# Performance work log

Hardware: AMD Instinct MI355X
Metric: run time of the kernel (lower is better)

## Reference

```python
import jax, jax.numpy as jnp
import numpy as np

L, E, S, V, B, T = 6, 768, 1024, 32000, 2, 1024
FF = 4 * E
EPS = 1e-5

def _layernorm(v, w, b):
    m = jnp.mean(v, axis=-1, keepdims=True)
    var = jnp.mean((v - m) ** 2, axis=-1, keepdims=True)
    return (v - m) * jax.lax.rsqrt(var + EPS) * w + b

def setup_inputs() -> dict:
    key = jax.random.key(0)
    ks = jax.random.split(key, 12)
    s = 0.02
    n = lambda k, shp: (jax.random.normal(k, shp, jnp.float32) * s)
    return {
        "x": jax.random.randint(ks[0], (B, T), 0, V),
        "tok_emb": n(ks[1], (V, E)),
        "pos_emb": jax.random.normal(ks[2], (S, E), jnp.float32),  # nn.Parameter(randn)
        "Wq": n(ks[3], (L, E, E)), "bq": jnp.zeros((L, E), jnp.float32),
        "Wk": n(ks[4], (L, E, E)), "bk": jnp.zeros((L, E), jnp.float32),
        "Wv": n(ks[5], (L, E, E)), "bv": jnp.zeros((L, E), jnp.float32),
        "ln1w": jnp.ones((L, E), jnp.float32), "ln1b": jnp.zeros((L, E), jnp.float32),
        "W1": n(ks[6], (L, E, FF)), "b1": jnp.zeros((L, FF), jnp.float32),
        "W2": n(ks[7], (L, FF, E)), "b2": jnp.zeros((L, E), jnp.float32),
        "ln2w": jnp.ones((L, E), jnp.float32), "ln2b": jnp.zeros((L, E), jnp.float32),
        "Wo": n(ks[8], (E, V)), "bo": jnp.zeros((V,), jnp.float32),
    }

def reference(x, tok_emb, pos_emb, Wq, bq, Wk, bk, Wv, bv, ln1w, ln1b,
              W1, b1, W2, b2, ln2w, ln2b, Wo, bo):
    t = x.shape[1]
    h = tok_emb[x] + pos_emb[:t]  # [B,T,E]
    scale = jnp.sqrt(jnp.float32(E))
    tril = jnp.tril(jnp.ones((t, t), bool))

    def layer(h, p):
        wq, bq_, wk, bk_, wv, bv_, l1w, l1b, w1, b1_, w2, b2_, l2w, l2b = p
        Q = h @ wq + bq_
        K = h @ wk + bk_
        Vv = h @ wv + bv_
        scores = jnp.einsum('btd,bsd->bts', Q, K) / scale
        # original adds a mask of 1.0 on allowed positions, -inf elsewhere
        masked = jnp.where(tril, scores + 1.0, -jnp.inf)
        A = jax.nn.softmax(masked, axis=-1)
        att = jnp.einsum('bts,bsd->btd', A, Vv)
        h1 = _layernorm(h + att, l1w, l1b)
        ffn = jax.nn.relu(h1 @ w1 + b1_) @ w2 + b2_
        h2 = _layernorm(ffn + h1, l2w, l2b)
        return h2, None

    params = (Wq, bq, Wk, bk, Wv, bv, ln1w, ln1b, W1, b1, W2, b2, ln2w, ln2b)
    h, _ = jax.lax.scan(layer, h, params)
    return h @ Wo + bo  # [B,T,V]
```

## Files before the change

kernel.cpp:

```cpp
#include <hip/hip_runtime.h>
#include <stdint.h>

typedef __bf16 v8bf __attribute__((ext_vector_type(8)));
typedef float  v4f  __attribute__((ext_vector_type(4)));

__device__ __forceinline__ float bf2f(uint16_t h) {
    union { uint32_t u; float f; } x; x.u = ((uint32_t)h) << 16; return x.f;
}
__device__ __forceinline__ uint16_t f2bf(float f) {
    union { float f; uint32_t u; } x; x.f = f;
    uint32_t r = x.u + 0x7fffu + ((x.u >> 16) & 1u);
    return (uint16_t)(r >> 16);
}

__device__ __forceinline__ void gload16(const uint16_t* g, uint16_t* l) {
    __builtin_amdgcn_global_load_lds((const __attribute__((address_space(1))) void*)g,
                                     (__attribute__((address_space(3))) void*)l, 16, 0, 0);
}

__global__ void k_embed(const int* __restrict__ x, const float* __restrict__ tok,
                        const float* __restrict__ pos, float* __restrict__ hf,
                        uint16_t* __restrict__ hb)
{
    int i = blockIdx.x;
    int t = i & 1023;
    int tk = x[i];
    const float* te = tok + (long)tk * 768;
    const float* pe = pos + (long)t * 768;
    for (int j = threadIdx.x; j < 768; j += 256) {
        float v = te[j] + pe[j];
        hf[(long)i * 768 + j] = v;
        hb[(long)i * 768 + j] = f2bf(v);
    }
}

template<typename SrcT>
__global__ void k_transpose(const SrcT* __restrict__ src, uint16_t* __restrict__ dst,
                            int ldS, int ldD, long sBatch, long dBatch)
{
    __shared__ float tile[32][33];
    src += (long)blockIdx.z * sBatch;
    dst += (long)blockIdx.z * dBatch;
    int c0 = blockIdx.x * 32, r0 = blockIdx.y * 32;
    int tx = threadIdx.x, ty = threadIdx.y;
    #pragma unroll
    for (int i = 0; i < 4; ++i) {
        int r = r0 + ty + i * 8;
        SrcT s = src[(long)r * ldS + c0 + tx];
        float v;
        if constexpr (sizeof(SrcT) == 4) v = (float)s; else v = bf2f((uint16_t)s);
        tile[ty + i * 8][tx] = v;
    }
    __syncthreads();
    #pragma unroll
    for (int i = 0; i < 4; ++i) {
        int c = c0 + ty + i * 8;
        dst[(long)c * ldD + r0 + tx] = f2bf(tile[tx][ty + i * 8]);
    }
}

__global__ void k_concat3(const float* __restrict__ a, const float* __restrict__ b,
                          const float* __restrict__ c, float* __restrict__ out)
{
    int l = blockIdx.y;
    const float* s = (blockIdx.x == 0) ? a : ((blockIdx.x == 1) ? b : c);
    s += (long)l * 768;
    for (int j = threadIdx.x; j < 768; j += 256)
        out[(long)l * 2304 + blockIdx.x * 768 + j] = s[j];
}

template<typename OutT, int BN, bool BIAS, bool RELU, bool RES>
__global__ void k_gemm(const uint16_t* __restrict__ A, const uint16_t* __restrict__ BT,
                       OutT* __restrict__ C, const float* __restrict__ bias,
                       const float* __restrict__ res,
                       int K, int lda, int ldb, int ldc,
                       long bsA, long bsB, long bsC, float scale, int causal)
{
    constexpr int NT = BN / 32;
    const int nwg = gridDim.x * gridDim.y;
    int lin = blockIdx.y * gridDim.x + blockIdx.x;
    {
        int q = nwg >> 3, r = nwg & 7, x = lin & 7, i = lin >> 3;
        lin = (x < r ? x * (q + 1) : r * (q + 1) + (x - r) * q) + i;
    }
    const int mt = lin % gridDim.y;
    const int nt = lin / gridDim.y;

    if (causal == 1 && nt * BN >= (mt + 1) * 128) return;
    const int Keff = (causal == 2) ? ((mt + 1) * 128 < K ? (mt + 1) * 128 : K) : K;

    __shared__ uint16_t As[128 * 32];
    __shared__ uint16_t Bs[BN * 32];
    const int tid  = threadIdx.x;
    const int lane = tid & 63;
    const int bz   = blockIdx.z;
    const uint16_t* Ab = A + (long)bz * bsA + (long)mt * 128 * lda;
    const uint16_t* Bb = BT + (long)bz * bsB + (long)nt * BN * ldb;

    const int wm = (tid >> 6) >> 1, wn = (tid >> 6) & 1;
    const int fr = lane & 15, fq = lane >> 4;

    const int r0 = tid >> 2;
    const int s0 = (tid & 3) * 8;

    v4f acc[4][NT];
    #pragma unroll
    for (int m = 0; m < 4; ++m)
        #pragma unroll
        for (int n = 0; n < NT; ++n) acc[m][n] = (v4f){0.f, 0.f, 0.f, 0.f};

    for (int kt = 0; kt < Keff; kt += 32) {
        gload16(Ab + (long)r0 * lda + kt + s0,        &As[tid * 8]);
        gload16(Ab + (long)(r0 + 64) * lda + kt + s0, &As[2048 + tid * 8]);
        gload16(Bb + (long)r0 * ldb + kt + s0,        &Bs[tid * 8]);
        if constexpr (BN == 128)
            gload16(Bb + (long)(r0 + 64) * ldb + kt + s0, &Bs[2048 + tid * 8]);
        __syncthreads();
        v8bf ag[4], bg[NT];
        #pragma unroll
        for (int m = 0; m < 4; ++m)
            ag[m] = *(const v8bf*)&As[(wm * 64 + m * 16 + fr) * 32 + fq * 8];
        #pragma unroll
        for (int n = 0; n < NT; ++n)
            bg[n] = *(const v8bf*)&Bs[(wn * (BN / 2) + n * 16 + fr) * 32 + fq * 8];
        #pragma unroll
        for (int m = 0; m < 4; ++m)
            #pragma unroll
            for (int n = 0; n < NT; ++n)
                acc[m][n] = __builtin_amdgcn_mfma_f32_16x16x32_bf16(ag[m], bg[n], acc[m][n], 0, 0, 0);
        __syncthreads();
    }

    OutT* Cb = C + (long)bz * bsC + (long)mt * 128 * ldc + nt * BN;
    const float* Rb = RES ? (res + (long)bz * bsC + (long)mt * 128 * ldc + nt * BN) : nullptr;
    #pragma unroll
    for (int n = 0; n < NT; ++n) {
        int col = wn * (BN / 2) + n * 16 + fr;
        float bv = BIAS ? bias[nt * BN + col] : 0.f;
        #pragma unroll
        for (int m = 0; m < 4; ++m) {
            #pragma unroll
            for (int r = 0; r < 4; ++r) {
                int row = wm * 64 + m * 16 + fq * 4 + r;
                float v = acc[m][n][r] * scale + bv;
                if (RES) v += Rb[(long)row * ldc + col];
                if (RELU) v = fmaxf(v, 0.f);
                if constexpr (sizeof(OutT) == 4) Cb[(long)row * ldc + col] = v;
                else                             Cb[(long)row * ldc + col] = f2bf(v);
            }
        }
    }
}

__global__ void k_softmax(const float* __restrict__ S, uint16_t* __restrict__ P)
{
    int t = blockIdx.x, b = blockIdx.y;
    const float* row = S + ((long)b * 1024 + t) * 1024;
    uint16_t* pr = P + ((long)b * 1024 + t) * 1024;
    int limit = (t & ~127) + 128;
    int s0 = threadIdx.x * 4;
    float vals[4] = {0.f, 0.f, 0.f, 0.f};
    if (s0 < limit) {
        float4 vv = *(const float4*)(row + s0);
        vals[0] = vv.x; vals[1] = vv.y; vals[2] = vv.z; vals[3] = vv.w;
    }
    float mx = -1e30f;
    #pragma unroll
    for (int j = 0; j < 4; ++j) if (s0 + j <= t) mx = fmaxf(mx, vals[j]);
    #pragma unroll
    for (int o = 32; o; o >>= 1) mx = fmaxf(mx, __shfl_xor(mx, o));
    __shared__ float red[8];
    int wave = threadIdx.x >> 6, lane = threadIdx.x & 63;
    if (lane == 0) red[wave] = mx;
    __syncthreads();
    mx = fmaxf(fmaxf(red[0], red[1]), fmaxf(red[2], red[3]));
    float e[4]; float sum = 0.f;
    #pragma unroll
    for (int j = 0; j < 4; ++j) { e[j] = (s0 + j <= t) ? __expf(vals[j] - mx) : 0.f; sum += e[j]; }
    #pragma unroll
    for (int o = 32; o; o >>= 1) sum += __shfl_xor(sum, o);
    if (lane == 0) red[4 + wave] = sum;
    __syncthreads();
    sum = red[4] + red[5] + red[6] + red[7];
    float inv = 1.f / sum;
    if (s0 < limit) {
        #pragma unroll
        for (int j = 0; j < 4; ++j) pr[s0 + j] = f2bf(e[j] * inv);
    }
}

__global__ void k_ln(const float* __restrict__ a,
                     const float* __restrict__ w, const float* __restrict__ bias,
                     float* __restrict__ outf, uint16_t* __restrict__ outb)
{
    int row = blockIdx.x;
    const float* ar = a + (long)row * 768;
    float v[3]; float s1 = 0.f, s2 = 0.f;
    #pragma unroll
    for (int i = 0; i < 3; ++i) {
        int e = threadIdx.x + i * 256;
        v[i] = ar[e];
        s1 += v[i]; s2 += v[i] * v[i];
    }
    #pragma unroll
    for (int o = 32; o; o >>= 1) { s1 += __shfl_xor(s1, o); s2 += __shfl_xor(s2, o); }
    __shared__ float red[8];
    int wave = threadIdx.x >> 6, lane = threadIdx.x & 63;
    if (lane == 0) { red[wave] = s1; red[4 + wave] = s2; }
    __syncthreads();
    s1 = red[0] + red[1] + red[2] + red[3];
    s2 = red[4] + red[5] + red[6] + red[7];
    float mean = s1 * (1.f / 768.f);
    float var  = s2 * (1.f / 768.f) - mean * mean;
    float rstd = rsqrtf(var + 1e-5f);
    #pragma unroll
    for (int i = 0; i < 3; ++i) {
        int e = threadIdx.x + i * 256;
        float o = (v[i] - mean) * rstd * w[e] + bias[e];
        outf[(long)row * 768 + e] = o;
        outb[(long)row * 768 + e] = f2bf(o);
    }
}

__global__ void k_ln_ffn2(const float* __restrict__ p, long pstride,
                          const float* __restrict__ b2, const float* __restrict__ h1,
                          const float* __restrict__ w, const float* __restrict__ bias,
                          float* __restrict__ outf, uint16_t* __restrict__ outb)
{
    int row = blockIdx.x;
    long base = (long)row * 768;
    float v[3]; float s1 = 0.f, s2 = 0.f;
    #pragma unroll
    for (int i = 0; i < 3; ++i) {
        int e = threadIdx.x + i * 256;
        float acc = b2[e] + h1[base + e];
        #pragma unroll
        for (int s = 0; s < 4; ++s) acc += p[base + e + s * pstride];
        v[i] = acc;
        s1 += acc; s2 += acc * acc;
    }
    #pragma unroll
    for (int o = 32; o; o >>= 1) { s1 += __shfl_xor(s1, o); s2 += __shfl_xor(s2, o); }
    __shared__ float red[8];
    int wave = threadIdx.x >> 6, lane = threadIdx.x & 63;
    if (lane == 0) { red[wave] = s1; red[4 + wave] = s2; }
    __syncthreads();
    s1 = red[0] + red[1] + red[2] + red[3];
    s2 = red[4] + red[5] + red[6] + red[7];
    float mean = s1 * (1.f / 768.f);
    float var  = s2 * (1.f / 768.f) - mean * mean;
    float rstd = rsqrtf(var + 1e-5f);
    #pragma unroll
    for (int i = 0; i < 3; ++i) {
        int e = threadIdx.x + i * 256;
        float o = (v[i] - mean) * rstd * w[e] + bias[e];
        outf[base + e] = o;
        outb[base + e] = f2bf(o);
    }
}

extern "C" void kernel_launch(void* const* d_in, const int* in_sizes, int n_in,
                              void* d_out, int out_size, void* d_ws, size_t ws_size,
                              hipStream_t stream)
{
    const int*   x       = (const int*)d_in[0];
    const float* tok_emb = (const float*)d_in[1];
    const float* pos_emb = (const float*)d_in[2];
    const float* Wq  = (const float*)d_in[3];
    const float* bq  = (const float*)d_in[4];
    const float* Wk  = (const float*)d_in[5];
    const float* bk  = (const float*)d_in[6];
    const float* Wv  = (const float*)d_in[7];
    const float* bv  = (const float*)d_in[8];
    const float* ln1w = (const float*)d_in[9];
    const float* ln1b = (const float*)d_in[10];
    const float* W1  = (const float*)d_in[11];
    const float* b1  = (const float*)d_in[12];
    const float* W2  = (const float*)d_in[13];
    const float* b2  = (const float*)d_in[14];
    const float* ln2w = (const float*)d_in[15];
    const float* ln2b = (const float*)d_in[16];
    const float* Wo  = (const float*)d_in[17];
    const float* bo  = (const float*)d_in[18];
    float* out = (float*)d_out;
    (void)in_sizes; (void)n_in; (void)out_size;

    char* ws = (char*)d_ws;
    size_t off = 0;
    auto alloc = [&](size_t bytes) -> char* {
        char* p = ws + off;
        off = (off + bytes + 255) & ~(size_t)255;
        return p;
    };
    uint16_t* WoT   = (uint16_t*)alloc(32000L * 768 * 2);
    float*    hf    = (float*)alloc(2048L * 768 * 4);
    uint16_t* hb    = (uint16_t*)alloc(2048L * 768 * 2);
    uint16_t* qkv   = (uint16_t*)alloc(2048L * 2304 * 2);
    uint16_t* vT    = (uint16_t*)alloc(2L * 768 * 1024 * 2);
    float*    sc    = (float*)alloc(2L * 1024 * 1024 * 4);
    uint16_t* pr    = (uint16_t*)alloc(2L * 1024 * 1024 * 2);
    float*    hsum  = (float*)alloc(2048L * 768 * 4);
    float*    h1f   = (float*)alloc(2048L * 768 * 4);
    uint16_t* h1b   = (uint16_t*)alloc(2048L * 768 * 2);
    uint16_t* f1    = (uint16_t*)alloc(2048L * 3072 * 2);
    float*    f2p   = (float*)alloc(4L * 2048 * 768 * 4);
    float*    bqkvA = (float*)alloc(6L * 2304 * 4);
    const long PSTR = 2048L * 768;

    size_t mark = off;
    uint16_t* WqkvTA = (uint16_t*)alloc(6L * 2304 * 768 * 2);
    uint16_t* W1TA   = (uint16_t*)alloc(6L * 3072 * 768 * 2);
    uint16_t* W2TA   = (uint16_t*)alloc(6L * 768 * 3072 * 2);
    bool hoist = (off <= ws_size);
    uint16_t *WqkvT = nullptr, *W1T = nullptr, *W2T = nullptr;
    if (!hoist) {
        off = mark;
        WqkvT = (uint16_t*)alloc(2304L * 768 * 2);
        W1T   = (uint16_t*)alloc(3072L * 768 * 2);
        W2T   = (uint16_t*)alloc(768L * 3072 * 2);
    }

    dim3 tb(32, 8);
    const float iscale = 0.036084391824351615f;
    const long EE = 768L * 768;

    k_transpose<float><<<dim3(1000, 24, 1), tb, 0, stream>>>(Wo, WoT, 32000, 768, 0, 0);
    k_embed<<<2048, 256, 0, stream>>>(x, tok_emb, pos_emb, hf, hb);
    k_concat3<<<dim3(3, 6), 256, 0, stream>>>(bq, bk, bv, bqkvA);

    if (hoist) {
        k_transpose<float><<<dim3(24, 24, 6), tb, 0, stream>>>(Wq, WqkvTA,             768, 768, EE, 2304L*768);
        k_transpose<float><<<dim3(24, 24, 6), tb, 0, stream>>>(Wk, WqkvTA + 768L*768,  768, 768, EE, 2304L*768);
        k_transpose<float><<<dim3(24, 24, 6), tb, 0, stream>>>(Wv, WqkvTA + 1536L*768, 768, 768, EE, 2304L*768);
        k_transpose<float><<<dim3(96, 24, 6), tb, 0, stream>>>(W1, W1TA, 3072, 768, 768L*3072, 3072L*768);
        k_transpose<float><<<dim3(24, 96, 6), tb, 0, stream>>>(W2, W2TA, 768, 3072, 3072L*768, 768L*3072);
    }

    for (int l = 0; l < 6; ++l) {
        uint16_t* WqkvL = hoist ? (WqkvTA + l * 2304L * 768) : WqkvT;
        uint16_t* W1L   = hoist ? (W1TA   + l * 3072L * 768) : W1T;
        uint16_t* W2L   = hoist ? (W2TA   + l * 768L * 3072) : W2T;
        if (!hoist) {
            k_transpose<float><<<dim3(24, 24, 1), tb, 0, stream>>>(Wq + l * EE, WqkvT,             768, 768, 0, 0);
            k_transpose<float><<<dim3(24, 24, 1), tb, 0, stream>>>(Wk + l * EE, WqkvT + 768L*768,  768, 768, 0, 0);
            k_transpose<float><<<dim3(24, 24, 1), tb, 0, stream>>>(Wv + l * EE, WqkvT + 1536L*768, 768, 768, 0, 0);
            k_transpose<float><<<dim3(96, 24, 1), tb, 0, stream>>>(W1 + l * 768L * 3072, W1T, 3072, 768, 0, 0);
            k_transpose<float><<<dim3(24, 96, 1), tb, 0, stream>>>(W2 + l * 3072L * 768, W2T, 768, 3072, 0, 0);
        }

        k_gemm<uint16_t, 64, true, false, false><<<dim3(36, 16, 1), 256, 0, stream>>>(
            hb, WqkvL, qkv, bqkvA + l * 2304, nullptr, 768, 768, 768, 2304, 0, 0, 0, 1.f, 0);
        k_gemm<float, 64, false, false, false><<<dim3(16, 8, 2), 256, 0, stream>>>(
            qkv, qkv + 768, sc, nullptr, nullptr, 768, 2304, 2304, 1024,
            1024L * 2304, 1024L * 2304, 1024L * 1024, iscale, 1);
        k_softmax<<<dim3(1024, 2), 256, 0, stream>>>(sc, pr);
        k_transpose<uint16_t><<<dim3(24, 32, 2), tb, 0, stream>>>(
            qkv + 1536, vT, 2304, 1024, 1024L * 2304, 768L * 1024);
        k_gemm<float, 64, false, false, true><<<dim3(12, 8, 2), 256, 0, stream>>>(
            pr, vT, hsum, nullptr, hf, 1024, 1024, 1024, 768,
            1024L * 1024, 768L * 1024, 1024L * 768, 1.f, 2);
        k_ln<<<2048, 256, 0, stream>>>(hsum, ln1w + l * 768, ln1b + l * 768, h1f, h1b);
        k_gemm<uint16_t, 64, true, true, false><<<dim3(48, 16, 1), 256, 0, stream>>>(
            h1b, W1L, f1, b1 + l * 3072, nullptr, 768, 768, 768, 3072, 0, 0, 0, 1.f, 0);
        k_gemm<float, 128, false, false, false><<<dim3(6, 16, 4), 256, 0, stream>>>(
            f1, W2L, f2p, nullptr, nullptr, 768, 3072, 3072, 768,
            768, 768, PSTR, 1.f, 0);
        k_ln_ffn2<<<2048, 256, 0, stream>>>(f2p, PSTR, b2 + l * 768, h1f,
                                            ln2w + l * 768, ln2b + l * 768, hf, hb);
    }

    k_gemm<float, 128, true, false, false><<<dim3(250, 16, 1), 256, 0, stream>>>(
        hb, WoT, out, bo, nullptr, 768, 768, 768, 32000, 0, 0, 0, 1.f, 0);
}
```

Before: 969.9 us.

## Add 256x256-tile pipelined GEMM for the vocabulary output projection

Adds a dedicated 512-thread GEMM kernel with 256x256 output tiles, a 4-slot LDS ring buffer loaded through global_load_lds with a two-stage prefetch distance, XOR swizzling, split A-half MFMA phases with s_setprio, and an XCD-aware workgroup remap. It replaces the previous 128-row-tile GEMM for the final 2048x768 by 768x32000 logits projection. The aim is more reuse per tile and overlap of loads with MFMA on the largest GEMM. The larger tile gives fewer workgroups (1000) and high register pressure from 32 accumulators per thread.

```diff
diff --git a/kernel.cpp b/kernel.cpp
--- a/kernel.cpp
+++ b/kernel.cpp
@@ -147,6 +147,116 @@
                 if (RELU) v = fmaxf(v, 0.f);
                 if constexpr (sizeof(OutT) == 4) Cb[(long)row * ldc + col] = v;
                 else                             Cb[(long)row * ldc + col] = f2bf(v);
+            }
+        }
+    }
+}
+
+__global__ __launch_bounds__(512, 2)
+void k_gemm256(const uint16_t* __restrict__ A, const uint16_t* __restrict__ BT,
+               float* __restrict__ C, const float* __restrict__ bias,
+               int K, int lda, int ldb, int ldc, float scale)
+{
+    __shared__ uint16_t lds[4][2][8192];
+
+    const int nwg = gridDim.x * gridDim.y;
+    int lin = blockIdx.y * gridDim.x + blockIdx.x;
+    {
+        int q = nwg >> 3, r = nwg & 7, x = lin & 7, i = lin >> 3;
+        lin = (x < r ? x * (q + 1) : r * (q + 1) + (x - r) * q) + i;
+    }
+    const int mt = lin % gridDim.y;
+    const int nt = lin / gridDim.y;
+
+    const int tid  = threadIdx.x;
+    const int lane = tid & 63;
+    const int wid  = tid >> 6;
+    const int wm = wid >> 2, wn = wid & 3;
+    const int fr = lane & 15, fq = lane >> 4;
+    const int swz = (fq ^ (fr & 3)) * 8;
+
+    const uint16_t* Ab = A  + (long)mt * 256 * lda;
+    const uint16_t* Bb = BT + (long)nt * 256 * ldb;
+
+    const int srow = tid >> 2;
+    const int ssl  = ((tid & 3) ^ (srow & 3)) * 8;
+    const int KT   = K >> 5;
+
+    v4f acc[8][4];
+    #pragma unroll
+    for (int m = 0; m < 8; ++m)
+        #pragma unroll
+        for (int n = 0; n < 4; ++n) acc[m][n] = (v4f){0.f, 0.f, 0.f, 0.f};
+
+    #pragma unroll
+    for (int t = 0; t < 2; ++t) {
+        gload16(Ab + (long)srow * lda + t * 32 + ssl,         &lds[t][0][tid * 8]);
+        gload16(Ab + (long)(srow + 128) * lda + t * 32 + ssl, &lds[t][0][4096 + tid * 8]);
+        gload16(Bb + (long)srow * ldb + t * 32 + ssl,         &lds[t][1][tid * 8]);
+        gload16(Bb + (long)(srow + 128) * ldb + t * 32 + ssl, &lds[t][1][4096 + tid * 8]);
+    }
+
+    for (int kti = 0; kti < KT; ++kti) {
+        const int ring = kti & 3;
+        const uint16_t* lA = &lds[ring][0][0];
+        const uint16_t* lB = &lds[ring][1][0];
+        uint16_t* sA = &lds[(ring + 2) & 3][0][0];
+        uint16_t* sB = &lds[(ring + 2) & 3][1][0];
+        const int koff = (kti + 2) * 32;
+        const bool more = (kti + 2) < KT;
+
+        if (kti + 1 < KT) asm volatile("s_waitcnt vmcnt(4)" ::: "memory");
+        else              asm volatile("s_waitcnt vmcnt(0)" ::: "memory");
+        __builtin_amdgcn_s_barrier();
+
+        v8bf bfr[4], a0[4];
+        #pragma unroll
+        for (int n = 0; n < 4; ++n)
+            bfr[n] = *(const v8bf*)&lB[(wn * 64 + n * 16 + fr) * 32 + swz];
+        #pragma unroll
+        for (int m = 0; m < 4; ++m)
+            a0[m] = *(const v8bf*)&lA[(wm * 128 + m * 16 + fr) * 32 + swz];
+        if (more) {
+            gload16(Ab + (long)srow * lda + koff + ssl,         &sA[tid * 8]);
+            gload16(Ab + (long)(srow + 128) * lda + koff + ssl, &sA[4096 + tid * 8]);
+        }
+        __builtin_amdgcn_s_setprio(1);
+        #pragma unroll
+        for (int m = 0; m < 4; ++m)
+            #pragma unroll
+            for (int n = 0; n < 4; ++n)
+                acc[m][n] = __builtin_amdgcn_mfma_f32_16x16x32_bf16(a0[m], bfr[n], acc[m][n], 0, 0, 0);
+        __builtin_amdgcn_s_setprio(0);
+
+        __builtin_amdgcn_s_barrier();
+        v8bf a1[4];
+        #pragma unroll
+        for (int m = 0; m < 4; ++m)
+            a1[m] = *(const v8bf*)&lA[(wm * 128 + (m + 4) * 16 + fr) * 32 + swz];
+        if (more) {
+            gload16(Bb + (long)srow * ldb + koff + ssl,         &sB[tid * 8]);
+            gload16(Bb + (long)(srow + 128) * ldb + koff + ssl, &sB[4096 + tid * 8]);
+        }
+        __builtin_amdgcn_s_setprio(1);
+        #pragma unroll
+        for (int m = 0; m < 4; ++m)
+            #pragma unroll
+            for (int n = 0; n < 4; ++n)
+                acc[m + 4][n] = __builtin_amdgcn_mfma_f32_16x16x32_bf16(a1[m], bfr[n], acc[m + 4][n], 0, 0, 0);
+        __builtin_amdgcn_s_setprio(0);
+    }
+
+    float* Cb = C + (long)(mt * 256 + wm * 128) * ldc + nt * 256 + wn * 64;
+    #pragma unroll
+    for (int n = 0; n < 4; ++n) {
+        int col = n * 16 + fr;
+        float bv = bias[nt * 256 + wn * 64 + col];
+        #pragma unroll
+        for (int m = 0; m < 8; ++m) {
+            #pragma unroll
+            for (int r = 0; r < 4; ++r) {
+                int row = m * 16 + fq * 4 + r;
+                Cb[(long)row * ldc + col] = acc[m][n][r] * scale + bv;
             }
         }
     }
@@ -369,6 +479,6 @@
                                             ln2w + l * 768, ln2b + l * 768, hf, hb);
     }
 
-    k_gemm<float, 128, true, false, false><<<dim3(250, 16, 1), 256, 0, stream>>>(
-        hb, WoT, out, bo, nullptr, 768, 768, 768, 32000, 0, 0, 0, 1.f, 0);
-}
+    k_gemm256<<<dim3(125, 8, 1), 512, 0, stream>>>(
+        hb, WoT, out, bo, 768, 768, 768, 32000, 1.f);
+}
```

Result: no change. 962.9 us (-0.7%).
